# Kernel optimization log

Measured on AMD Instinct MI355X. Metric: run time of the kernel, lower is better.

## Reference

```python
import jax, jax.numpy as jnp
import numpy as np

NUM_HEADS = 16
EPS = 1e-5


def _layernorm(x, w):
    # torch LayerNorm (biased variance), bias=False
    m = jnp.mean(x, axis=-1, keepdims=True)
    v = jnp.mean(jnp.square(x - m), axis=-1, keepdims=True)
    return (x - m) * jax.lax.rsqrt(v + EPS) * w


def setup_inputs() -> dict:
    key = jax.random.key(0)
    ks = jax.random.split(key, 8)
    B, S, H, A = 2, 2048, 1024, 1024
    hd = H // NUM_HEADS
    return {
        "x": jax.random.normal(ks[0], (B, S, H), jnp.float32),
        "ada_cond": jax.random.normal(ks[1], (B, A), jnp.float32),
        "freqs": jax.random.normal(ks[2], (S, hd // 2, 2), jnp.float32),
        "w_qkv": jax.random.normal(ks[3], (3 * H, H), jnp.float32) * (1.0 / np.sqrt(H)),
        "w_o": jax.random.normal(ks[4], (H, H), jnp.float32) * (1.0 / np.sqrt(H)),
        "ln_w": jnp.ones((H,), jnp.float32),
        "mod_w": jax.random.normal(ks[5], (3 * H, A), jnp.float32) * 0.02,
        "mod_b": jax.random.normal(ks[6], (3 * H,), jnp.float32) * 0.02,
        "qn_w": jnp.ones((hd,), jnp.float32),
        "kn_w": jnp.ones((hd,), jnp.float32),
    }


def reference(x, ada_cond, freqs, w_qkv, w_o, ln_w, mod_w, mod_b, qn_w, kn_w):
    B, S, H = x.shape
    nh = NUM_HEADS
    hd = H // nh

    # pre-norm + AdaLN modulation (with gate)
    h = _layernorm(x, ln_w)
    mod = (jax.nn.silu(ada_cond) @ mod_w.T + mod_b)[:, None, :]  # [B,1,3H]
    scale, shift, gate = jnp.split(mod, 3, axis=-1)
    h = h * (scale + 1.0) + shift

    # QKV projection and head split
    qkv = h @ w_qkv.T                                  # [B,S,3H]
    q, k, v = jnp.split(qkv, 3, axis=-1)
    to_heads = lambda t: t.reshape(B, S, nh, hd).transpose(0, 2, 1, 3)  # [B,nh,S,hd]
    q, k, v = to_heads(q), to_heads(k), to_heads(v)

    # per-head QK layernorm
    q = _layernorm(q, qn_w)
    k = _layernorm(k, kn_w)

    # RoPE (complex rotation via interleaved pairs)
    f = freqs[:S].reshape(1, 1, S, hd // 2, 2)

    def rope(t):
        tr = t.reshape(B, nh, S, hd // 2, 2)
        re = tr[..., 0] * f[..., 0] - tr[..., 1] * f[..., 1]
        im = tr[..., 1] * f[..., 0] + tr[..., 0] * f[..., 1]
        return jnp.stack([re, im], axis=-1).reshape(B, nh, S, hd)

    q, k = rope(q), rope(k)

    # scaled dot-product attention (non-causal)
    scores = jnp.einsum("bhqd,bhkd->bhqk", q, k) * (1.0 / np.sqrt(hd))
    attn = jax.nn.softmax(scores, axis=-1)
    o = jnp.einsum("bhqk,bhkd->bhqd", attn, v)
    o = o.transpose(0, 2, 1, 3).reshape(B, S, H)

    return (o @ w_o.T) * gate
```

## Files before the change

kernel.cpp:

```cpp
#include <hip/hip_runtime.h>
#include <hip/hip_bf16.h>
#include <math.h>

#define B_ 2
#define S_ 2048
#define H_ 1024
#define A_ 1024
#define NH_ 16
#define HD_ 64
#define H3_ 3072
#define EPS_ 1e-5f

typedef __attribute__((ext_vector_type(8))) short short8;
typedef __attribute__((ext_vector_type(4))) float floatx4;

__device__ inline unsigned short f2bf(float x) {
    union { float f; unsigned u; } v; v.f = x;
    unsigned r = v.u + 0x7fffu + ((v.u >> 16) & 1u);
    return (unsigned short)(r >> 16);
}

__device__ inline unsigned pk_bf16(float a, float b) {
    union { __hip_bfloat162 h; unsigned u; } v;
    v.h = __float22bfloat162_rn(make_float2(a, b));
    return v.u;
}

__device__ inline void gld_lds16(const void* g, void* l) {
    __builtin_amdgcn_global_load_lds(
        (const __attribute__((address_space(1))) unsigned int*)g,
        (__attribute__((address_space(3))) unsigned int*)l, 16, 0, 0);
}

#define TBLK(r) ((((r) >> 3) * 544) + (((r) & 7) * 64))

__global__ __launch_bounds__(256) void cast_bf16_kernel(
    const float* __restrict__ in, unsigned short* __restrict__ out, int n)
{
    int i = (blockIdx.x * 256 + threadIdx.x) * 8;
    if (i >= n) return;
    float4 a = *(const float4*)(in + i);
    float4 b = *(const float4*)(in + i + 4);
    uint4 o;
    o.x = pk_bf16(a.x, a.y);
    o.y = pk_bf16(a.z, a.w);
    o.z = pk_bf16(b.x, b.y);
    o.w = pk_bf16(b.z, b.w);
    *(uint4*)(out + i) = o;
}

__global__ __launch_bounds__(256) void mod_gemv_kernel(
    const float* __restrict__ ada, const float* __restrict__ mod_w,
    const float* __restrict__ mod_b, float* __restrict__ mod)
{
    int wid = threadIdx.x >> 6;
    int lane = threadIdx.x & 63;
    int idx = blockIdx.x * 4 + wid;
    int b = idx / H3_;
    int j = idx % H3_;
    const float* ar = ada + (size_t)b * A_;
    const float* wr = mod_w + (size_t)j * A_;
    float acc = 0.f;
    for (int a = lane; a < A_; a += 64) {
        float av = ar[a];
        float sv = av / (1.f + __expf(-av));
        acc += sv * wr[a];
    }
    #pragma unroll
    for (int m = 1; m < 64; m <<= 1) acc += __shfl_xor(acc, m);
    if (lane == 0) mod[idx] = acc + mod_b[j];
}

__global__ __launch_bounds__(256) void ln_mod_kernel(
    const float* __restrict__ x, const float* __restrict__ ln_w,
    const float* __restrict__ mod, unsigned short* __restrict__ hout)
{
    int row = blockIdx.x;
    int b = row >> 11;
    const float* xr = x + (size_t)row * H_;
    int t = threadIdx.x;
    float4 xv = *(const float4*)(xr + t * 4);
    float s1 = xv.x + xv.y + xv.z + xv.w;
    float s2 = xv.x*xv.x + xv.y*xv.y + xv.z*xv.z + xv.w*xv.w;
    #pragma unroll
    for (int m = 1; m < 64; m <<= 1) { s1 += __shfl_xor(s1, m); s2 += __shfl_xor(s2, m); }
    __shared__ float r1[4], r2[4];
    int wid = t >> 6, lane = t & 63;
    if (lane == 0) { r1[wid] = s1; r2[wid] = s2; }
    __syncthreads();
    s1 = r1[0] + r1[1] + r1[2] + r1[3];
    s2 = r2[0] + r2[1] + r2[2] + r2[3];
    float mean = s1 * (1.f / H_);
    float var  = s2 * (1.f / H_) - mean * mean;
    float rstd = rsqrtf(var + EPS_);
    const float* mrow = mod + (size_t)b * H3_;
    float4 wv = *(const float4*)(ln_w + t * 4);
    float4 sc = *(const float4*)(mrow + t * 4);
    float4 sh = *(const float4*)(mrow + H_ + t * 4);
    float4 hv;
    hv.x = (xv.x - mean) * rstd * wv.x * (sc.x + 1.f) + sh.x;
    hv.y = (xv.y - mean) * rstd * wv.y * (sc.y + 1.f) + sh.y;
    hv.z = (xv.z - mean) * rstd * wv.z * (sc.z + 1.f) + sh.z;
    hv.w = (xv.w - mean) * rstd * wv.w * (sc.w + 1.f) + sh.w;
    uint2 o;
    o.x = pk_bf16(hv.x, hv.y);
    o.y = pk_bf16(hv.z, hv.w);
    *(uint2*)(hout + (size_t)row * H_ + t * 4) = o;
}

__global__ __launch_bounds__(256) void gemm_bt_bf16_kernel(
    const unsigned short* __restrict__ A, const unsigned short* __restrict__ Bm,
    float* __restrict__ C, int M, int N, int K,
    const float* __restrict__ gate, int gate_stride, int batch_shift)
{
    __shared__ unsigned short As[128 * 32];
    __shared__ unsigned short Bs[128 * 32];
    int t = threadIdx.x;
    int w = t >> 6, lane = t & 63;
    int q16 = lane & 15, quad = lane >> 4;
    int wm = w >> 1, wn = w & 1;
    int m0 = blockIdx.y * 128, n0 = blockIdx.x * 128;

    int srow = (w << 5) + (lane >> 2);
    int soff = (lane & 3) << 3;
    const unsigned short* ga = A + (size_t)(m0 + srow) * K + soff;
    const unsigned short* gb = Bm + (size_t)(n0 + srow) * K + soff;
    unsigned short* la0 = As + (w << 5) * 32;
    unsigned short* la1 = la0 + 16 * 32;
    unsigned short* lb0 = Bs + (w << 5) * 32;
    unsigned short* lb1 = lb0 + 16 * 32;

    floatx4 acc[4][4];
    #pragma unroll
    for (int mt = 0; mt < 4; ++mt)
        #pragma unroll
        for (int nt = 0; nt < 4; ++nt)
            acc[mt][nt] = (floatx4){0.f, 0.f, 0.f, 0.f};

    int a_row = wm * 64 + q16;
    int b_row = wn * 64 + q16;

    for (int kt = 0; kt < K; kt += 32) {
        __syncthreads();
        gld_lds16(ga, la0);
        gld_lds16(ga + (size_t)16 * K, la1);
        gld_lds16(gb, lb0);
        gld_lds16(gb + (size_t)16 * K, lb1);
        ga += 32; gb += 32;
        __syncthreads();

        short8 af[4], bf[4];
        #pragma unroll
        for (int mt = 0; mt < 4; ++mt)
            af[mt] = *(const short8*)&As[(a_row + mt * 16) * 32 + quad * 8];
        #pragma unroll
        for (int nt = 0; nt < 4; ++nt)
            bf[nt] = *(const short8*)&Bs[(b_row + nt * 16) * 32 + quad * 8];
        #pragma unroll
        for (int mt = 0; mt < 4; ++mt)
            #pragma unroll
            for (int nt = 0; nt < 4; ++nt)
                acc[mt][nt] = __builtin_amdgcn_mfma_f32_16x16x32_bf16(
                    af[mt], bf[nt], acc[mt][nt], 0, 0, 0);
    }

    #pragma unroll
    for (int mt = 0; mt < 4; ++mt) {
        #pragma unroll
        for (int i = 0; i < 4; ++i) {
            int m = m0 + wm * 64 + mt * 16 + quad * 4 + i;
            float* crow = C + (size_t)m * N;
            const float* grow = gate ? gate + (size_t)(m >> batch_shift) * gate_stride
                                     : nullptr;
            #pragma unroll
            for (int nt = 0; nt < 4; ++nt) {
                int n = n0 + wn * 64 + nt * 16 + q16;
                float v = acc[mt][nt][i];
                if (gate) v *= grow[n];
                crow[n] = v;
            }
        }
    }
}

__global__ __launch_bounds__(256) void qk_ln_rope_kernel(
    const float* __restrict__ qkv, const float* __restrict__ freqs,
    const float* __restrict__ qn_w, const float* __restrict__ kn_w,
    unsigned short* __restrict__ qout, unsigned short* __restrict__ kout,
    unsigned short* __restrict__ vtout)
{
    __shared__ unsigned short vt_lds[64][72];
    int t = threadIdx.x;
    int w = t >> 6, lane = t & 63;
    int bh = blockIdx.x >> 5;
    int sblk = blockIdx.x & 31;
    int h = bh & (NH_ - 1);
    int b = bh >> 4;

    float qnw = qn_w[lane], knw = kn_w[lane];

    for (int it = 0; it < 16; ++it) {
        int s_local = w * 16 + it;
        int s = sblk * 64 + s_local;
        const float* base = qkv + ((size_t)(b * S_ + s)) * H3_;
        float qv = base[h * HD_ + lane];
        float kv = base[H_ + h * HD_ + lane];
        float vv = base[2 * H_ + h * HD_ + lane];

        float qs1 = qv, qs2 = qv * qv, ks1 = kv, ks2 = kv * kv;
        #pragma unroll
        for (int m = 1; m < 64; m <<= 1) {
            qs1 += __shfl_xor(qs1, m); qs2 += __shfl_xor(qs2, m);
            ks1 += __shfl_xor(ks1, m); ks2 += __shfl_xor(ks2, m);
        }
        float qm = qs1 * (1.f / 64), qvar = qs2 * (1.f / 64) - qm * qm;
        float km = ks1 * (1.f / 64), kvar = ks2 * (1.f / 64) - km * km;
        qv = (qv - qm) * rsqrtf(qvar + EPS_) * qnw;
        kv = (kv - km) * rsqrtf(kvar + EPS_) * knw;

        float f0 = freqs[(size_t)s * 64 + (lane >> 1) * 2 + 0];
        float f1 = freqs[(size_t)s * 64 + (lane >> 1) * 2 + 1];
        float qp = __shfl_xor(qv, 1);
        float kp = __shfl_xor(kv, 1);
        float qr = (lane & 1) ? (qv * f0 + qp * f1) : (qv * f0 - qp * f1);
        float kr = (lane & 1) ? (kv * f0 + kp * f1) : (kv * f0 - kp * f1);

        size_t o = ((size_t)bh * S_ + s) * HD_ + lane;
        qout[o] = f2bf(qr * 0.1803368801111244f);
        kout[o] = f2bf(kr);
        vt_lds[lane][s_local] = f2bf(vv);
    }
    __syncthreads();
    for (int i = t; i < 512; i += 256) {
        int r = i >> 3, c8 = i & 7;
        *(uint4*)(vtout + ((size_t)bh * 64 + r) * S_ + sblk * 64 + c8 * 8) =
            *(const uint4*)&vt_lds[r][c8 * 8];
    }
}

__global__ __launch_bounds__(256) void attn_mfma_kernel(
    const unsigned short* __restrict__ q, const unsigned short* __restrict__ k,
    const unsigned short* __restrict__ vt, unsigned short* __restrict__ o)
{
    __shared__ unsigned short Ks[8 * 544];
    __shared__ unsigned short Vs[8 * 544];
    __shared__ unsigned short Ps[4][16][72];

    int t = threadIdx.x;
    int w = t >> 6, lane = t & 63;
    int q16 = lane & 15, quad = lane >> 4;
    int bh = blockIdx.y, b = bh >> 4, h = bh & 15;
    int s0 = blockIdx.x * 64;

    const unsigned short* qg = q + ((size_t)bh * S_ + s0) * HD_;
    gld_lds16(qg + (2 * w) * 512 + lane * 8, &Ks[(2 * w) * 544]);
    gld_lds16(qg + (2 * w + 1) * 512 + lane * 8, &Ks[(2 * w + 1) * 544]);
    __syncthreads();
    int qrow = TBLK(16 * w + q16);
    short8 qf0 = *(const short8*)&Ks[qrow + quad * 8];
    short8 qf1 = *(const short8*)&Ks[qrow + 32 + quad * 8];

    short8 ones8;
    #pragma unroll
    for (int i = 0; i < 8; ++i) ones8[i] = (short)0x3F80;

    floatx4 acc_o[4];
    floatx4 acc_l = (floatx4){0.f, 0.f, 0.f, 0.f};
    #pragma unroll
    for (int i = 0; i < 4; ++i) acc_o[i] = (floatx4){0.f, 0.f, 0.f, 0.f};

    const unsigned short* kg = k + (size_t)bh * S_ * HD_;
    const unsigned short* vg = vt + (size_t)bh * 64 * S_;
    int vsrc = (16 * w + (lane >> 3)) * S_ + (lane & 7) * 8;

    for (int kt = 0; kt < S_ / 64; ++kt) {
        __syncthreads();
        gld_lds16(kg + (2 * w) * 512 + lane * 8, &Ks[(2 * w) * 544]);
        gld_lds16(kg + (2 * w + 1) * 512 + lane * 8, &Ks[(2 * w + 1) * 544]);
        gld_lds16(vg + vsrc, &Vs[(2 * w) * 544]);
        gld_lds16(vg + vsrc + 8 * S_, &Vs[(2 * w + 1) * 544]);
        kg += 64 * HD_;
        vg += 64;
        __syncthreads();

        floatx4 sc[4];
        #pragma unroll
        for (int nk = 0; nk < 4; ++nk) sc[nk] = (floatx4){-12.f, -12.f, -12.f, -12.f};
        #pragma unroll
        for (int nk = 0; nk < 4; ++nk) {
            int krow = TBLK(16 * nk + q16);
            short8 kf0 = *(const short8*)&Ks[krow + quad * 8];
            short8 kf1 = *(const short8*)&Ks[krow + 32 + quad * 8];
            sc[nk] = __builtin_amdgcn_mfma_f32_16x16x32_bf16(kf0, qf0, sc[nk], 0, 0, 0);
            sc[nk] = __builtin_amdgcn_mfma_f32_16x16x32_bf16(kf1, qf1, sc[nk], 0, 0, 0);
        }

        #pragma unroll
        for (int nk = 0; nk < 4; ++nk) {
            float p0 = exp2f(sc[nk][0]);
            float p1 = exp2f(sc[nk][1]);
            float p2 = exp2f(sc[nk][2]);
            float p3 = exp2f(sc[nk][3]);
            uint2 pk;
            pk.x = pk_bf16(p0, p1);
            pk.y = pk_bf16(p2, p3);
            *(uint2*)&Ps[w][q16][16 * nk + quad * 4] = pk;
        }

        __asm__ __volatile__("" ::: "memory");

        #pragma unroll
        for (int ks = 0; ks < 2; ++ks) {
            short8 pf = *(const short8*)&Ps[w][q16][ks * 32 + quad * 8];
            acc_l = __builtin_amdgcn_mfma_f32_16x16x32_bf16(ones8, pf, acc_l, 0, 0, 0);
            #pragma unroll
            for (int nd = 0; nd < 4; ++nd) {
                short8 vf = *(const short8*)&Vs[TBLK(16 * nd + q16) + ks * 32 + quad * 8];
                acc_o[nd] = __builtin_amdgcn_mfma_f32_16x16x32_bf16(vf, pf, acc_o[nd], 0, 0, 0);
            }
        }
    }

    float inv = 1.f / acc_l[0];
    #pragma unroll
    for (int nd = 0; nd < 4; ++nd) {
        uint2 pk;
        pk.x = pk_bf16(acc_o[nd][0] * inv, acc_o[nd][1] * inv);
        pk.y = pk_bf16(acc_o[nd][2] * inv, acc_o[nd][3] * inv);
        *(uint2*)&Ps[w][q16][16 * nd + quad * 4] = pk;
    }
    __asm__ __volatile__("" ::: "memory");
    unsigned short* og = o + ((size_t)(b * S_ + s0 + 16 * w + q16)) * H_ + h * HD_;
    #pragma unroll
    for (int i = 0; i < 2; ++i) {
        int c = quad * 2 + i;
        *(short8*)(og + c * 8) = *(const short8*)&Ps[w][q16][c * 8];
    }
}

extern "C" void kernel_launch(void* const* d_in, const int* in_sizes, int n_in,
                              void* d_out, int out_size, void* d_ws, size_t ws_size,
                              hipStream_t stream)
{
    const float* x     = (const float*)d_in[0];
    const float* ada   = (const float*)d_in[1];
    const float* freqs = (const float*)d_in[2];
    const float* w_qkv = (const float*)d_in[3];
    const float* w_o   = (const float*)d_in[4];
    const float* ln_w  = (const float*)d_in[5];
    const float* mod_w = (const float*)d_in[6];
    const float* mod_b = (const float*)d_in[7];
    const float* qn_w  = (const float*)d_in[8];
    const float* kn_w  = (const float*)d_in[9];
    float* out = (float*)d_out;

    float* ws  = (float*)d_ws;
    float* mod = ws;
    float* qkv = mod + 8192;
    unsigned short* hb    = (unsigned short*)(qkv + (size_t)B_ * S_ * H3_);
    unsigned short* qb    = hb + (size_t)B_ * S_ * H_;
    unsigned short* kb    = qb + (size_t)B_ * S_ * H_;
    unsigned short* vtb   = kb + (size_t)B_ * S_ * H_;
    unsigned short* ob    = vtb + (size_t)B_ * S_ * H_;
    unsigned short* wqkvb = ob + (size_t)B_ * S_ * H_;
    unsigned short* wob   = wqkvb + (size_t)H3_ * H_;

    cast_bf16_kernel<<<H3_ * H_ / (8 * 256), 256, 0, stream>>>(w_qkv, wqkvb, H3_ * H_);
    cast_bf16_kernel<<<H_ * H_ / (8 * 256), 256, 0, stream>>>(w_o, wob, H_ * H_);
    mod_gemv_kernel<<<B_ * H3_ / 4, 256, 0, stream>>>(ada, mod_w, mod_b, mod);
    ln_mod_kernel<<<B_ * S_, 256, 0, stream>>>(x, ln_w, mod, hb);
    gemm_bt_bf16_kernel<<<dim3(H3_ / 128, B_ * S_ / 128), 256, 0, stream>>>(
        hb, wqkvb, qkv, B_ * S_, H3_, H_, nullptr, 0, 0);
    qk_ln_rope_kernel<<<B_ * NH_ * S_ / 64, 256, 0, stream>>>(
        qkv, freqs, qn_w, kn_w, qb, kb, vtb);
    attn_mfma_kernel<<<dim3(S_ / 64, B_ * NH_), 256, 0, stream>>>(qb, kb, vtb, ob);
    gemm_bt_bf16_kernel<<<dim3(H_ / 128, B_ * S_ / 128), 256, 0, stream>>>(
        ob, wob, out, B_ * S_, H_, H_, mod + 2 * H_, H3_, 11);
}
```

Measured before the change: 283.3 us.

## Fuse QK layernorm, RoPE and V transpose into QKV GEMM epilogue

The QKV GEMM epilogue now does per-head layernorm of Q and K with a 16-lane shuffle reduction, applies RoPE and the softmax scale, and writes bf16 Q/K plus a transposed V directly. This removes the separate qk_ln_rope kernel and the fp32 qkv round trip through global memory. The V transpose is written with strided 8-byte stores, which may coalesce poorly. The attention softmax also switches to the hardware exp2 builtin to avoid the library wrapper.

Result: faster. 270.0 us (-4.7%).

```diff
diff --git a/kernel.cpp b/kernel.cpp
--- a/kernel.cpp
+++ b/kernel.cpp
@@ -108,13 +108,15 @@
     *(uint2*)(hout + (size_t)row * H_ + t * 4) = o;
 }
 
-__global__ __launch_bounds__(256) void gemm_bt_bf16_kernel(
+__global__ __launch_bounds__(256) void gemm_qkv_fused_kernel(
     const unsigned short* __restrict__ A, const unsigned short* __restrict__ Bm,
-    float* __restrict__ C, int M, int N, int K,
-    const float* __restrict__ gate, int gate_stride, int batch_shift)
+    const float* __restrict__ freqs, const float* __restrict__ qn_w,
+    const float* __restrict__ kn_w, unsigned short* __restrict__ qout,
+    unsigned short* __restrict__ kout, unsigned short* __restrict__ vtout)
 {
     __shared__ unsigned short As[128 * 32];
     __shared__ unsigned short Bs[128 * 32];
+    const int K = H_, N = H3_;
     int t = threadIdx.x;
     int w = t >> 6, lane = t & 63;
     int q16 = lane & 15, quad = lane >> 4;
@@ -164,6 +166,129 @@
                     af[mt], bf[nt], acc[mt][nt], 0, 0, 0);
     }
 
+    int n_base = n0 + wn * 64;
+    int sec = n_base >> 10;
+    int head = (n_base & 1023) >> 6;
+
+    if (sec == 2) {
+        #pragma unroll
+        for (int mt = 0; mt < 4; ++mt) {
+            int m = m0 + wm * 64 + mt * 16 + quad * 4;
+            int b = m >> 11, s = m & (S_ - 1);
+            #pragma unroll
+            for (int nt = 0; nt < 4; ++nt) {
+                int d = nt * 16 + q16;
+                unsigned short* dst =
+                    vtout + ((size_t)((b * 16 + head) * 64 + d)) * S_ + s;
+                uint2 pk;
+                pk.x = pk_bf16(acc[mt][nt][0], acc[mt][nt][1]);
+                pk.y = pk_bf16(acc[mt][nt][2], acc[mt][nt][3]);
+                *(uint2*)dst = pk;
+            }
+        }
+    } else {
+        const float* nw = (sec == 0) ? qn_w : kn_w;
+        float w4[4];
+        #pragma unroll
+        for (int nt = 0; nt < 4; ++nt) w4[nt] = nw[nt * 16 + q16];
+        unsigned short* outp = (sec == 0) ? qout : kout;
+        float qscale = (sec == 0) ? 0.1803368801111244f : 1.0f;
+
+        #pragma unroll
+        for (int mt = 0; mt < 4; ++mt) {
+            #pragma unroll
+            for (int i = 0; i < 4; ++i) {
+                int m = m0 + wm * 64 + mt * 16 + quad * 4 + i;
+                int b = m >> 11, s = m & (S_ - 1);
+                float v0 = acc[mt][0][i], v1 = acc[mt][1][i];
+                float v2 = acc[mt][2][i], v3 = acc[mt][3][i];
+                float s1 = (v0 + v1) + (v2 + v3);
+                float s2 = (v0 * v0 + v1 * v1) + (v2 * v2 + v3 * v3);
+                #pragma unroll
+                for (int msk = 1; msk < 16; msk <<= 1) {
+                    s1 += __shfl_xor(s1, msk);
+                    s2 += __shfl_xor(s2, msk);
+                }
+                float mean = s1 * (1.f / 64);
+                float var  = s2 * (1.f / 64) - mean * mean;
+                float rstd = rsqrtf(var + EPS_);
+                float vv[4];
+                vv[0] = (v0 - mean) * rstd * w4[0];
+                vv[1] = (v1 - mean) * rstd * w4[1];
+                vv[2] = (v2 - mean) * rstd * w4[2];
+                vv[3] = (v3 - mean) * rstd * w4[3];
+                const float* fr = freqs + (size_t)s * 64;
+                unsigned short* orow = outp + ((size_t)((b * 16 + head) * S_ + s)) * 64;
+                #pragma unroll
+                for (int nt = 0; nt < 4; ++nt) {
+                    int c = nt * 16 + q16;
+                    float vp = __shfl_xor(vv[nt], 1);
+                    float2 ff = *(const float2*)(fr + (c & ~1));
+                    float r = (c & 1) ? (vv[nt] * ff.x + vp * ff.y)
+                                      : (vv[nt] * ff.x - vp * ff.y);
+                    orow[c] = f2bf(r * qscale);
+                }
+            }
+        }
+    }
+}
+
+__global__ __launch_bounds__(256) void gemm_bt_bf16_kernel(
+    const unsigned short* __restrict__ A, const unsigned short* __restrict__ Bm,
+    float* __restrict__ C, int M, int N, int K,
+    const float* __restrict__ gate, int gate_stride, int batch_shift)
+{
+    __shared__ unsigned short As[128 * 32];
+    __shared__ unsigned short Bs[128 * 32];
+    int t = threadIdx.x;
+    int w = t >> 6, lane = t & 63;
+    int q16 = lane & 15, quad = lane >> 4;
+    int wm = w >> 1, wn = w & 1;
+    int m0 = blockIdx.y * 128, n0 = blockIdx.x * 128;
+
+    int srow = (w << 5) + (lane >> 2);
+    int soff = (lane & 3) << 3;
+    const unsigned short* ga = A + (size_t)(m0 + srow) * K + soff;
+    const unsigned short* gb = Bm + (size_t)(n0 + srow) * K + soff;
+    unsigned short* la0 = As + (w << 5) * 32;
+    unsigned short* la1 = la0 + 16 * 32;
+    unsigned short* lb0 = Bs + (w << 5) * 32;
+    unsigned short* lb1 = lb0 + 16 * 32;
+
+    floatx4 acc[4][4];
+    #pragma unroll
+    for (int mt = 0; mt < 4; ++mt)
+        #pragma unroll
+        for (int nt = 0; nt < 4; ++nt)
+            acc[mt][nt] = (floatx4){0.f, 0.f, 0.f, 0.f};
+
+    int a_row = wm * 64 + q16;
+    int b_row = wn * 64 + q16;
+
+    for (int kt = 0; kt < K; kt += 32) {
+        __syncthreads();
+        gld_lds16(ga, la0);
+        gld_lds16(ga + (size_t)16 * K, la1);
+        gld_lds16(gb, lb0);
+        gld_lds16(gb + (size_t)16 * K, lb1);
+        ga += 32; gb += 32;
+        __syncthreads();
+
+        short8 af[4], bf[4];
+        #pragma unroll
+        for (int mt = 0; mt < 4; ++mt)
+            af[mt] = *(const short8*)&As[(a_row + mt * 16) * 32 + quad * 8];
+        #pragma unroll
+        for (int nt = 0; nt < 4; ++nt)
+            bf[nt] = *(const short8*)&Bs[(b_row + nt * 16) * 32 + quad * 8];
+        #pragma unroll
+        for (int mt = 0; mt < 4; ++mt)
+            #pragma unroll
+            for (int nt = 0; nt < 4; ++nt)
+                acc[mt][nt] = __builtin_amdgcn_mfma_f32_16x16x32_bf16(
+                    af[mt], bf[nt], acc[mt][nt], 0, 0, 0);
+    }
+
     #pragma unroll
     for (int mt = 0; mt < 4; ++mt) {
         #pragma unroll
@@ -180,61 +305,6 @@
                 crow[n] = v;
             }
         }
-    }
-}
-
-__global__ __launch_bounds__(256) void qk_ln_rope_kernel(
-    const float* __restrict__ qkv, const float* __restrict__ freqs,
-    const float* __restrict__ qn_w, const float* __restrict__ kn_w,
-    unsigned short* __restrict__ qout, unsigned short* __restrict__ kout,
-    unsigned short* __restrict__ vtout)
-{
-    __shared__ unsigned short vt_lds[64][72];
-    int t = threadIdx.x;
-    int w = t >> 6, lane = t & 63;
-    int bh = blockIdx.x >> 5;
-    int sblk = blockIdx.x & 31;
-    int h = bh & (NH_ - 1);
-    int b = bh >> 4;
-
-    float qnw = qn_w[lane], knw = kn_w[lane];
-
-    for (int it = 0; it < 16; ++it) {
-        int s_local = w * 16 + it;
-        int s = sblk * 64 + s_local;
-        const float* base = qkv + ((size_t)(b * S_ + s)) * H3_;
-        float qv = base[h * HD_ + lane];
-        float kv = base[H_ + h * HD_ + lane];
-        float vv = base[2 * H_ + h * HD_ + lane];
-
-        float qs1 = qv, qs2 = qv * qv, ks1 = kv, ks2 = kv * kv;
-        #pragma unroll
-        for (int m = 1; m < 64; m <<= 1) {
-            qs1 += __shfl_xor(qs1, m); qs2 += __shfl_xor(qs2, m);
-            ks1 += __shfl_xor(ks1, m); ks2 += __shfl_xor(ks2, m);
-        }
-        float qm = qs1 * (1.f / 64), qvar = qs2 * (1.f / 64) - qm * qm;
-        float km = ks1 * (1.f / 64), kvar = ks2 * (1.f / 64) - km * km;
-        qv = (qv - qm) * rsqrtf(qvar + EPS_) * qnw;
-        kv = (kv - km) * rsqrtf(kvar + EPS_) * knw;
-
-        float f0 = freqs[(size_t)s * 64 + (lane >> 1) * 2 + 0];
-        float f1 = freqs[(size_t)s * 64 + (lane >> 1) * 2 + 1];
-        float qp = __shfl_xor(qv, 1);
-        float kp = __shfl_xor(kv, 1);
-        float qr = (lane & 1) ? (qv * f0 + qp * f1) : (qv * f0 - qp * f1);
-        float kr = (lane & 1) ? (kv * f0 + kp * f1) : (kv * f0 - kp * f1);
-
-        size_t o = ((size_t)bh * S_ + s) * HD_ + lane;
-        qout[o] = f2bf(qr * 0.1803368801111244f);
-        kout[o] = f2bf(kr);
-        vt_lds[lane][s_local] = f2bf(vv);
-    }
-    __syncthreads();
-    for (int i = t; i < 512; i += 256) {
-        int r = i >> 3, c8 = i & 7;
-        *(uint4*)(vtout + ((size_t)bh * 64 + r) * S_ + sblk * 64 + c8 * 8) =
-            *(const uint4*)&vt_lds[r][c8 * 8];
     }
 }
 
@@ -297,10 +367,10 @@
 
         #pragma unroll
         for (int nk = 0; nk < 4; ++nk) {
-            float p0 = exp2f(sc[nk][0]);
-            float p1 = exp2f(sc[nk][1]);
-            float p2 = exp2f(sc[nk][2]);
-            float p3 = exp2f(sc[nk][3]);
+            float p0 = __builtin_amdgcn_exp2f(sc[nk][0]);
+            float p1 = __builtin_amdgcn_exp2f(sc[nk][1]);
+            float p2 = __builtin_amdgcn_exp2f(sc[nk][2]);
+            float p3 = __builtin_amdgcn_exp2f(sc[nk][3]);
             uint2 pk;
             pk.x = pk_bf16(p0, p1);
             pk.y = pk_bf16(p2, p3);
@@ -356,8 +426,7 @@
 
     float* ws  = (float*)d_ws;
     float* mod = ws;
-    float* qkv = mod + 8192;
-    unsigned short* hb    = (unsigned short*)(qkv + (size_t)B_ * S_ * H3_);
+    unsigned short* hb    = (unsigned short*)(mod + 8192);
     unsigned short* qb    = hb + (size_t)B_ * S_ * H_;
     unsigned short* kb    = qb + (size_t)B_ * S_ * H_;
     unsigned short* vtb   = kb + (size_t)B_ * S_ * H_;
@@ -369,10 +438,8 @@
     cast_bf16_kernel<<<H_ * H_ / (8 * 256), 256, 0, stream>>>(w_o, wob, H_ * H_);
     mod_gemv_kernel<<<B_ * H3_ / 4, 256, 0, stream>>>(ada, mod_w, mod_b, mod);
     ln_mod_kernel<<<B_ * S_, 256, 0, stream>>>(x, ln_w, mod, hb);
-    gemm_bt_bf16_kernel<<<dim3(H3_ / 128, B_ * S_ / 128), 256, 0, stream>>>(
-        hb, wqkvb, qkv, B_ * S_, H3_, H_, nullptr, 0, 0);
-    qk_ln_rope_kernel<<<B_ * NH_ * S_ / 64, 256, 0, stream>>>(
-        qkv, freqs, qn_w, kn_w, qb, kb, vtb);
+    gemm_qkv_fused_kernel<<<dim3(H3_ / 128, B_ * S_ / 128), 256, 0, stream>>>(
+        hb, wqkvb, freqs, qn_w, kn_w, qb, kb, vtb);
     attn_mfma_kernel<<<dim3(S_ / 64, B_ * NH_), 256, 0, stream>>>(qb, kb, vtb, ob);
     gemm_bt_bf16_kernel<<<dim3(H_ / 128, B_ * S_ / 128), 256, 0, stream>>>(
         ob, wob, out, B_ * S_, H_, H_, mod + 2 * H_, H3_, 11);
```
